# Performance work log

Measured on AMD Instinct MI355X. Metric: run time of the kernel, lower is better.

The kernel has to match this reference:

```python
import jax, jax.numpy as jnp
import numpy as np

H, D = 4, 32          # heads, per-head dim (= hidden_channels)
HD = H * D            # concat width fed between layers
L = 2                 # num HGT layers
OUT = 128             # final output dim
SCALE = 1.0 / np.sqrt(D)


def _seg_softmax(score, seg, n):
    # segment softmax over incoming edges per destination node, per head
    mx = jax.ops.segment_max(score, seg, num_segments=n)
    ex = jnp.exp(score - mx[seg])
    den = jax.ops.segment_sum(ex, seg, num_segments=n)
    return ex / den[seg]


def _hgt_side(q_dst, k_src, v_src, src, dst, a_rel, m_rel, p_rel, n_dst):
    # k/v: [N_src,H,D]; a_rel,m_rel: [H,D,D]; p_rel: [H]
    k_t = jnp.einsum('ehd,hdf->ehf', k_src[src], a_rel)          # [E,H,D]
    score = (q_dst[dst] * k_t).sum(-1) * p_rel * SCALE           # [E,H]
    alpha = _seg_softmax(score, dst, n_dst)                      # [E,H]
    v_t = jnp.einsum('ehd,hdf->ehf', v_src[src], m_rel)          # [E,H,D]
    return jax.ops.segment_sum(alpha[..., None] * v_t, dst, num_segments=n_dst)


def _forward(x_m, x_g, W_in_m, b_in_m, W_in_g, b_in_g,
             Wk_m, bk_m, Wq_m, bq_m, Wv_m, bv_m,
             Wk_g, bk_g, Wq_g, bq_g, Wv_g, bv_g,
             a_mg, m_mg, p_mg, a_gm, m_gm, p_gm,
             Wa_m, ba_m, Wa_g, ba_g, skip_m, skip_g,
             W_out_m, b_out_m, W_out_g, b_out_g,
             edge_mg_src, edge_mg_dst, edge_gm_src, edge_gm_dst):
    Nm, Ng = x_m.shape[0], x_g.shape[0]
    # per-node-type input projection
    h_m = x_m @ W_in_m + b_in_m                                  # [Nm,HD]
    h_g = x_g @ W_in_g + b_in_g                                  # [Ng,HD]
    for l in range(L):
        k_m = (h_m @ Wk_m[l] + bk_m[l]).reshape(Nm, H, D)
        q_m = (h_m @ Wq_m[l] + bq_m[l]).reshape(Nm, H, D)
        v_m = (h_m @ Wv_m[l] + bv_m[l]).reshape(Nm, H, D)
        k_g = (h_g @ Wk_g[l] + bk_g[l]).reshape(Ng, H, D)
        q_g = (h_g @ Wq_g[l] + bq_g[l]).reshape(Ng, H, D)
        v_g = (h_g @ Wv_g[l] + bv_g[l]).reshape(Ng, H, D)
        agg_g = _hgt_side(q_g, k_m, v_m, edge_mg_src, edge_mg_dst,
                          a_mg[l], m_mg[l], p_mg[l], Ng)         # [Ng,H,D]
        agg_m = _hgt_side(q_m, k_g, v_g, edge_gm_src, edge_gm_dst,
                          a_gm[l], m_gm[l], p_gm[l], Nm)         # [Nm,H,D]
        o_m = jax.nn.gelu(agg_m.reshape(Nm, HD), approximate=False) @ Wa_m[l] + ba_m[l]
        o_g = jax.nn.gelu(agg_g.reshape(Ng, HD), approximate=False) @ Wa_g[l] + ba_g[l]
        bm = jax.nn.sigmoid(skip_m[l])
        bg = jax.nn.sigmoid(skip_g[l])
        h_m = jax.nn.elu(bm * o_m + (1.0 - bm) * h_m)            # HGTConv skip, then model-level ELU
        h_g = jax.nn.elu(bg * o_g + (1.0 - bg) * h_g)
    out_m = h_m @ W_out_m + b_out_m                              # [Nm,OUT]
    out_g = h_g @ W_out_g + b_out_g                              # [Ng,OUT]
    return jnp.concatenate([out_m, out_g], axis=0)               # [Nm+Ng,OUT]


def setup_inputs() -> dict:
    key = jax.random.key(0)
    ks = iter(jax.random.split(key, 64))
    Nm, Ng, E = 100000, 20000, 500000
    Fm, Fg = 20, 50
    def n(shape, s=0.05):
        return jax.random.normal(next(ks), shape, jnp.float32) * s
    inp = {
        'x_m': n((Nm, Fm), 1.0), 'x_g': n((Ng, Fg), 1.0),
        'W_in_m': n((Fm, HD)), 'b_in_m': jnp.zeros((HD,), jnp.float32),
        'W_in_g': n((Fg, HD)), 'b_in_g': jnp.zeros((HD,), jnp.float32),
        'Wk_m': n((L, HD, HD)), 'bk_m': jnp.zeros((L, HD), jnp.float32),
        'Wq_m': n((L, HD, HD)), 'bq_m': jnp.zeros((L, HD), jnp.float32),
        'Wv_m': n((L, HD, HD)), 'bv_m': jnp.zeros((L, HD), jnp.float32),
        'Wk_g': n((L, HD, HD)), 'bk_g': jnp.zeros((L, HD), jnp.float32),
        'Wq_g': n((L, HD, HD)), 'bq_g': jnp.zeros((L, HD), jnp.float32),
        'Wv_g': n((L, HD, HD)), 'bv_g': jnp.zeros((L, HD), jnp.float32),
        'a_mg': n((L, H, D, D)), 'm_mg': n((L, H, D, D)),
        'p_mg': jnp.ones((L, H), jnp.float32),
        'a_gm': n((L, H, D, D)), 'm_gm': n((L, H, D, D)),
        'p_gm': jnp.ones((L, H), jnp.float32),
        'Wa_m': n((L, HD, HD)), 'ba_m': jnp.zeros((L, HD), jnp.float32),
        'Wa_g': n((L, HD, HD)), 'ba_g': jnp.zeros((L, HD), jnp.float32),
        'skip_m': jnp.ones((L,), jnp.float32), 'skip_g': jnp.ones((L,), jnp.float32),
        'W_out_m': n((HD, OUT)), 'b_out_m': jnp.zeros((OUT,), jnp.float32),
        'W_out_g': n((HD, OUT)), 'b_out_g': jnp.zeros((OUT,), jnp.float32),
        'edge_mg_src': jax.random.randint(next(ks), (E,), 0, Nm, jnp.int32),
        'edge_mg_dst': jax.random.randint(next(ks), (E,), 0, Ng, jnp.int32),
        'edge_gm_src': jax.random.randint(next(ks), (E,), 0, Ng, jnp.int32),
        'edge_gm_dst': jax.random.randint(next(ks), (E,), 0, Nm, jnp.int32),
    }
    return inp


def reference(x_m, x_g, W_in_m, b_in_m, W_in_g, b_in_g,
              Wk_m, bk_m, Wq_m, bq_m, Wv_m, bv_m,
              Wk_g, bk_g, Wq_g, bq_g, Wv_g, bv_g,
              a_mg, m_mg, p_mg, a_gm, m_gm, p_gm,
              Wa_m, ba_m, Wa_g, ba_g, skip_m, skip_g,
              W_out_m, b_out_m, W_out_g, b_out_g,
              edge_mg_src, edge_mg_dst, edge_gm_src, edge_gm_dst):
    return _forward(x_m, x_g, W_in_m, b_in_m, W_in_g, b_in_g,
                    Wk_m, bk_m, Wq_m, bq_m, Wv_m, bv_m,
                    Wk_g, bk_g, Wq_g, bq_g, Wv_g, bv_g,
                    a_mg, m_mg, p_mg, a_gm, m_gm, p_gm,
                    Wa_m, ba_m, Wa_g, ba_g, skip_m, skip_g,
                    W_out_m, b_out_m, W_out_g, b_out_g,
                    edge_mg_src, edge_mg_dst, edge_gm_src, edge_gm_dst)
```

## Files before the change

kernel.cpp:

```cpp
#include <hip/hip_runtime.h>
#include <hip/hip_bf16.h>

#define SCALE_F 0.17677669529663688f

typedef __attribute__((ext_vector_type(8)))  short bfrag;
typedef __attribute__((ext_vector_type(16))) float facc;
typedef __attribute__((ext_vector_type(2)))  float f32x2;

extern "C" __device__ float __ocml_native_exp2_f32(float);

__device__ __forceinline__ float lo16(unsigned u){ return __uint_as_float(u << 16); }
__device__ __forceinline__ float hi16(unsigned u){ return __uint_as_float(u & 0xffff0000u); }
__device__ __forceinline__ float bu2f(unsigned short u){ return __uint_as_float((unsigned)u << 16); }
__device__ __forceinline__ unsigned short f2bu(float f){
    __hip_bfloat16 h = __float2bfloat16(f);
    return *reinterpret_cast<unsigned short*>(&h);
}
__device__ __forceinline__ void storeC(float* p, float v){ *p = v; }
__device__ __forceinline__ void storeC(__hip_bfloat16* p, float v){ *p = __float2bfloat16(v); }

__global__ void hist2_k(const int* __restrict__ d1, int* __restrict__ c1, int E1, int N1,
                        const int* __restrict__ d2, int* __restrict__ c2, int E2, int N2){
    const int* d = blockIdx.y ? d2 : d1;
    int* c = blockIdx.y ? c2 : c1;
    int E = blockIdx.y ? E2 : E1;
    int Nd = blockIdx.y ? N2 : N1;
    int e = blockIdx.x*256 + threadIdx.x;
    if (e >= E) return;
    int dd = d[e];
    if ((unsigned)dd < (unsigned)Nd) atomicAdd(&c[dd], 1);
}

__global__ void scan_block2_k(const int* __restrict__ c1, int* __restrict__ i1, int* __restrict__ b1, int N1,
                              const int* __restrict__ c2, int* __restrict__ i2, int* __restrict__ b2, int N2){
    const int* cnt = blockIdx.y ? c2 : c1;
    int* incl = blockIdx.y ? i2 : i1;
    int* bsum = blockIdx.y ? b2 : b1;
    int N = blockIdx.y ? N2 : N1;
    if ((int)blockIdx.x*256 >= N) return;
    __shared__ int sh[256];
    int tid = threadIdx.x;
    int i = blockIdx.x*256 + tid;
    int v = (i < N) ? cnt[i] : 0;
    sh[tid] = v;
    __syncthreads();
    for (int off = 1; off < 256; off <<= 1){
        int t = (tid >= off) ? sh[tid-off] : 0;
        __syncthreads();
        sh[tid] += t;
        __syncthreads();
    }
    if (i < N) incl[i] = sh[tid];
    if (tid == 255) bsum[blockIdx.x] = sh[255];
}

__global__ void scan_top2_k(int* __restrict__ b1, int nb1, int* __restrict__ b2, int nb2){
    int* bsum = blockIdx.x ? b2 : b1;
    int nb = blockIdx.x ? nb2 : nb1;
    __shared__ int sh[512];
    int tid = threadIdx.x;
    int v = (tid < nb) ? bsum[tid] : 0;
    sh[tid] = v;
    __syncthreads();
    for (int off = 1; off < 512; off <<= 1){
        int t = (tid >= off) ? sh[tid-off] : 0;
        __syncthreads();
        sh[tid] += t;
        __syncthreads();
    }
    if (tid < nb) bsum[tid] = sh[tid] - v;
}

__global__ void finalize2_k(const int* __restrict__ i1, const int* __restrict__ c1,
                            const int* __restrict__ b1, int* __restrict__ p1, int N1, int E1,
                            const int* __restrict__ i2, const int* __restrict__ c2,
                            const int* __restrict__ b2, int* __restrict__ p2, int N2, int E2){
    const int* incl = blockIdx.y ? i2 : i1;
    const int* cnt  = blockIdx.y ? c2 : c1;
    const int* boff = blockIdx.y ? b2 : b1;
    int* indptr = blockIdx.y ? p2 : p1;
    int N = blockIdx.y ? N2 : N1;
    int E = blockIdx.y ? E2 : E1;
    int i = blockIdx.x*256 + threadIdx.x;
    if (i > N) return;
    if (i == N){ indptr[N] = E; return; }
    indptr[i] = boff[i >> 8] + incl[i] - cnt[i];
}

__global__ void scatter2_k(const int* __restrict__ s1, const int* __restrict__ d1,
                           const int* __restrict__ p1, int* __restrict__ u1,
                           int* __restrict__ r1, int E1, int N1,
                           const int* __restrict__ s2, const int* __restrict__ d2,
                           const int* __restrict__ p2, int* __restrict__ u2,
                           int* __restrict__ r2, int E2, int N2){
    const int* src = blockIdx.y ? s2 : s1;
    const int* dst = blockIdx.y ? d2 : d1;
    const int* indptr = blockIdx.y ? p2 : p1;
    int* cur = blockIdx.y ? u2 : u1;
    int* csr = blockIdx.y ? r2 : r1;
    int E = blockIdx.y ? E2 : E1;
    int Nd = blockIdx.y ? N2 : N1;
    int e = blockIdx.x*256 + threadIdx.x;
    if (e >= E) return;
    int d = dst[e];
    if ((unsigned)d >= (unsigned)Nd) return;
    int p = indptr[d] + atomicAdd(&cur[d], 1);
    csr[p] = src[e];
}

template<int K>
__device__ __forceinline__ void in_proj_body(const float* __restrict__ x,
                                             const float* __restrict__ W,
                                             const float* __restrict__ b,
                                             unsigned short* __restrict__ h, int N){
    constexpr int KP4 = (K + 3)/4, KP = KP4*4;
    int j = threadIdx.x;
    float wreg[KP];
    #pragma unroll
    for (int k = 0; k < KP; ++k) wreg[k] = (k < K) ? W[k*128 + j] : 0.f;
    float bj = b[j];
    __shared__ float xs[8][KP];
    for (int base = blockIdx.x*8; base < N; base += gridDim.x*8){
        __syncthreads();
        for (int t = threadIdx.x; t < 8*KP; t += 128){
            int r = t / KP, k = t - r*KP;
            int row = base + r;
            xs[r][k] = (row < N && k < K) ? x[(size_t)row*K + k] : 0.f;
        }
        __syncthreads();
        #pragma unroll
        for (int r = 0; r < 8; ++r){
            int row = base + r;
            if (row >= N) break;
            float acc = bj;
            #pragma unroll
            for (int kk = 0; kk < KP4; ++kk){
                float4 xv = *(const float4*)(&xs[r][kk*4]);
                acc += xv.x*wreg[kk*4] + xv.y*wreg[kk*4+1]
                     + xv.z*wreg[kk*4+2] + xv.w*wreg[kk*4+3];
            }
            h[(size_t)row*128 + j] = f2bu(acc);
        }
    }
}

__global__ __launch_bounds__(128) void in_proj2_k(
    const float* __restrict__ xm, const float* __restrict__ Wm,
    const float* __restrict__ bm_, unsigned short* __restrict__ hm, int Nm,
    const float* __restrict__ xg, const float* __restrict__ Wg,
    const float* __restrict__ bg_, unsigned short* __restrict__ hg, int Ng){
    if (blockIdx.y == 0) in_proj_body<20>(xm, Wm, bm_, hm, Nm);
    else                 in_proj_body<50>(xg, Wg, bg_, hg, Ng);
}

__global__ __launch_bounds__(128) void wprep_k(
    const float* __restrict__ Wq_m, const float* __restrict__ bq_m,
    const float* __restrict__ Wk_m, const float* __restrict__ bk_m,
    const float* __restrict__ Wv_m, const float* __restrict__ bv_m,
    const float* __restrict__ a_mg, const float* __restrict__ m_mg,
    const float* __restrict__ Wq_g, const float* __restrict__ bq_g,
    const float* __restrict__ Wk_g, const float* __restrict__ bk_g,
    const float* __restrict__ Wv_g, const float* __restrict__ bv_g,
    const float* __restrict__ a_gm, const float* __restrict__ m_gm,
    unsigned short* __restrict__ Wtf, float* __restrict__ bfv,
    const float* __restrict__ Wa_m, const float* __restrict__ Wa_g,
    const float* __restrict__ W_out_m, const float* __restrict__ W_out_g,
    unsigned short* __restrict__ Wta, unsigned short* __restrict__ Wtout){
    int b = blockIdx.x;
    if (b < 1536){
        int u = b / 384, j = b % 384;
        int l = u >> 1;  bool sg = (u & 1);
        const float* Wq = (sg ? Wq_g : Wq_m) + l*16384;
        const float* bq = (sg ? bq_g : bq_m) + l*128;
        const float* Wk = (sg ? Wk_g : Wk_m) + l*16384;
        const float* bk = (sg ? bk_g : bk_m) + l*128;
        const float* Wv = (sg ? Wv_g : Wv_m) + l*16384;
        const float* bv = (sg ? bv_g : bv_m) + l*128;
        const float* ar = (sg ? a_gm : a_mg) + l*4096;
        const float* mr = (sg ? m_gm : m_mg) + l*4096;
        unsigned short* Wt = Wtf + (size_t)u*49152;
        float* bf = bfv + u*384;
        int row = threadIdx.x;
        int part = j >> 7, f = j & 127, hh = f >> 5, ff = f & 31;
        float v;
        if (part == 0) v = Wq[row*128 + f];
        else {
            const float* Wx  = (part == 1) ? Wk : Wv;
            const float* rel = (part == 1) ? ar : mr;
            float s = 0.f;
            #pragma unroll
            for (int d = 0; d < 32; ++d)
                s += Wx[row*128 + hh*32 + d] * rel[hh*1024 + d*32 + ff];
            v = s;
        }
        Wt[(size_t)j*128 + row] = f2bu(v);
        if (row == 0){
            float bb;
            if (part == 0) bb = bq[f];
            else {
                const float* bx  = (part == 1) ? bk : bv;
                const float* rel = (part == 1) ? ar : mr;
                float s = 0.f;
                for (int d = 0; d < 32; ++d)
                    s += bx[hh*32 + d] * rel[hh*1024 + d*32 + ff];
                bb = s;
            }
            bf[j] = bb;
        }
    } else {
        int t = b - 1536;
        int y = t >> 7;
        int idx = (t & 127)*128 + threadIdx.x;
        const float* S = (y==0)?Wa_m:(y==1)?Wa_g:(y==2)?(Wa_m+16384):(y==3)?(Wa_g+16384)
                        :(y==4)?W_out_m:W_out_g;
        unsigned short* D = (y==0)?Wta:(y==1)?(Wta+16384):(y==2)?(Wta+32768):(y==3)?(Wta+49152)
                           :(y==4)?Wtout:(Wtout+16384);
        int n = idx >> 7, k = idx & 127;
        D[idx] = f2bu(S[k*128 + n]);
    }
}

template<typename CT, int MODE, int NCHUNK>
__global__ __launch_bounds__(256) void mfma_gemm2(
    const unsigned short* __restrict__ A0, const unsigned short* __restrict__ Wt0,
    const float* __restrict__ bias0, CT* __restrict__ C0, unsigned short* __restrict__ H0,
    int N0, const float* __restrict__ skip0,
    const unsigned short* __restrict__ A1, const unsigned short* __restrict__ Wt1,
    const float* __restrict__ bias1, CT* __restrict__ C1, unsigned short* __restrict__ H1,
    int N1, const float* __restrict__ skip1,
    int ldc, int nblk0){
    bool s0 = ((int)blockIdx.x < nblk0);
    const unsigned short* A  = s0 ? A0 : A1;
    const unsigned short* Wt = s0 ? Wt0 : Wt1;
    const float* bias = s0 ? bias0 : bias1;
    CT* C = s0 ? C0 : C1;
    unsigned short* H = s0 ? H0 : H1;
    int N = s0 ? N0 : N1;
    const float* skip = s0 ? skip0 : skip1;
    int bx = s0 ? blockIdx.x : (blockIdx.x - nblk0);

    __shared__ unsigned short As[64][136];
    __shared__ unsigned short Bs[128][136];
    int tid = threadIdx.x;
    int rb = bx*64;
    #pragma unroll
    for (int ph = 0; ph < 4; ++ph){
        int c = ph*256 + tid;
        int r = c >> 4, off = (c & 15)*8;
        uint4 v = make_uint4(0,0,0,0);
        if (rb + r < N) v = ((const uint4*)(A + (size_t)(rb + r)*128))[c & 15];
        *(uint4*)(&As[r][off]) = v;
    }
    int w = tid >> 6, lane = tid & 63;
    int wr = (w >> 1)*32, wc = (w & 1)*64;
    int m = lane & 31, quad = lane >> 5;
    const unsigned short* ap  = &As[wr + m][quad*8];
    const unsigned short* bp0 = &Bs[wc + m][quad*8];
    const unsigned short* bp1 = &Bs[wc + 32 + m][quad*8];
    float bm = 0.f;
    if (MODE == 2) bm = 1.f/(1.f + __expf(-skip[0]));

    #pragma unroll
    for (int chunk = 0; chunk < NCHUNK; ++chunk){
        int cb = chunk*128;
        if (chunk > 0) __syncthreads();
        #pragma unroll
        for (int ph = 0; ph < 8; ++ph){
            int c = ph*256 + tid;
            int r = c >> 4, off = (c & 15)*8;
            uint4 v = ((const uint4*)(Wt + (size_t)(cb + r)*128))[c & 15];
            *(uint4*)(&Bs[r][off]) = v;
        }
        __syncthreads();
        facc acc0, acc1;
        #pragma unroll
        for (int i = 0; i < 16; ++i){ acc0[i] = 0.f; acc1[i] = 0.f; }
        #pragma unroll
        for (int kc = 0; kc < 8; ++kc){
            bfrag a  = *(const bfrag*)(ap  + kc*16);
            bfrag b0 = *(const bfrag*)(bp0 + kc*16);
            bfrag b1 = *(const bfrag*)(bp1 + kc*16);
            acc0 = __builtin_amdgcn_mfma_f32_32x32x16_bf16(a, b0, acc0, 0, 0, 0);
            acc1 = __builtin_amdgcn_mfma_f32_32x32x16_bf16(a, b1, acc1, 0, 0, 0);
        }
        int col0 = cb + wc + m, col1 = col0 + 32;
        float bias0v = bias[col0], bias1v = bias[col1];
        #pragma unroll
        for (int r = 0; r < 16; ++r){
            int lrow = wr + 4*quad + (r & 3) + 8*(r >> 2);
            int grow = rb + lrow;
            if (grow >= N) continue;
            float o0 = acc0[r] + bias0v;
            float o1 = acc1[r] + bias1v;
            if (MODE == 0){
                storeC(&C[(size_t)grow*ldc + col0], o0);
                storeC(&C[(size_t)grow*ldc + col1], o1);
            } else if (MODE == 1){
                unsigned short* qp = (unsigned short*)C;
                if (col0 < 128){
                    qp[(size_t)grow*128 + col0] = f2bu(o0);
                    qp[(size_t)grow*128 + col1] = f2bu(o1);
                } else {
                    H[(size_t)grow*256 + (col0 - 128)] = f2bu(o0);
                    H[(size_t)grow*256 + (col1 - 128)] = f2bu(o1);
                }
            } else {
                size_t i0 = (size_t)grow*128 + col0, i1 = (size_t)grow*128 + col1;
                float v0 = bm*o0 + (1.f - bm)*bu2f(H[i0]);
                float v1 = bm*o1 + (1.f - bm)*bu2f(H[i1]);
                v0 = (v0 > 0.f) ? v0 : expm1f(v0);
                v1 = (v1 > 0.f) ? v1 : expm1f(v1);
                H[i0] = f2bu(v0);
                H[i1] = f2bu(v1);
            }
        }
    }
}

__global__ __launch_bounds__(256) void mfma_fused_mid_k(
    const unsigned short* __restrict__ A0, const unsigned short* __restrict__ Wt0,
    const float* __restrict__ bias0, unsigned short* __restrict__ H0,
    const float* __restrict__ skip0, const unsigned short* __restrict__ Wf0,
    const float* __restrict__ bf0, unsigned short* __restrict__ q0,
    unsigned short* __restrict__ kv0, int N0,
    const unsigned short* __restrict__ A1, const unsigned short* __restrict__ Wt1,
    const float* __restrict__ bias1, unsigned short* __restrict__ H1,
    const float* __restrict__ skip1, const unsigned short* __restrict__ Wf1,
    const float* __restrict__ bf1, unsigned short* __restrict__ q1,
    unsigned short* __restrict__ kv1, int N1,
    int nblk0){
    bool s0 = ((int)blockIdx.x < nblk0);
    const unsigned short* A  = s0 ? A0 : A1;
    const unsigned short* Wt = s0 ? Wt0 : Wt1;
    const float* bias = s0 ? bias0 : bias1;
    unsigned short* H = s0 ? H0 : H1;
    const float* skip = s0 ? skip0 : skip1;
    const unsigned short* Wf = s0 ? Wf0 : Wf1;
    const float* bf = s0 ? bf0 : bf1;
    unsigned short* q = s0 ? q0 : q1;
    unsigned short* kv = s0 ? kv0 : kv1;
    int N = s0 ? N0 : N1;
    int bx = s0 ? blockIdx.x : (blockIdx.x - nblk0);

    __shared__ unsigned short As[64][136];
    __shared__ unsigned short Bs[128][136];
    int tid = threadIdx.x;
    int rb = bx*64;
    #pragma unroll
    for (int ph = 0; ph < 4; ++ph){
        int c = ph*256 + tid;
        int r = c >> 4, off = (c & 15)*8;
        uint4 v = make_uint4(0,0,0,0);
        if (rb + r < N) v = ((const uint4*)(A + (size_t)(rb + r)*128))[c & 15];
        *(uint4*)(&As[r][off]) = v;
    }
    #pragma unroll
    for (int ph = 0; ph < 8; ++ph){
        int c = ph*256 + tid;
        int r = c >> 4, off = (c & 15)*8;
        uint4 v = ((const uint4*)(Wt + (size_t)r*128))[c & 15];
        *(uint4*)(&Bs[r][off]) = v;
    }
    __syncthreads();
    int w = tid >> 6, lane = tid & 63;
    int wr = (w >> 1)*32, wc = (w & 1)*64;
    int m = lane & 31, quad = lane >> 5;
    const unsigned short* ap  = &As[wr + m][quad*8];
    const unsigned short* bp0 = &Bs[wc + m][quad*8];
    const unsigned short* bp1 = &Bs[wc + 32 + m][quad*8];
    float bm = 1.f/(1.f + __expf(-skip[0]));

    facc acc0, acc1;
    #pragma unroll
    for (int i = 0; i < 16; ++i){ acc0[i] = 0.f; acc1[i] = 0.f; }
    #pragma unroll
    for (int kc = 0; kc < 8; ++kc){
        bfrag a  = *(const bfrag*)(ap  + kc*16);
        bfrag b0 = *(const bfrag*)(bp0 + kc*16);
        bfrag b1 = *(const bfrag*)(bp1 + kc*16);
        acc0 = __builtin_amdgcn_mfma_f32_32x32x16_bf16(a, b0, acc0, 0, 0, 0);
        acc1 = __builtin_amdgcn_mfma_f32_32x32x16_bf16(a, b1, acc1, 0, 0, 0);
    }
    __syncthreads();

    #pragma unroll
    for (int ph = 0; ph < 8; ++ph){
        int c = ph*256 + tid;
        int r = c >> 4, off = (c & 15)*8;
        uint4 v = ((const uint4*)(Wf + (size_t)r*128))[c & 15];
        *(uint4*)(&Bs[r][off]) = v;
    }
    {
        int col0 = wc + m, col1 = col0 + 32;
        float bias0v = bias[col0], bias1v = bias[col1];
        #pragma unroll
        for (int r = 0; r < 16; ++r){
            int lrow = wr + 4*quad + (r & 3) + 8*(r >> 2);
            int grow = rb + lrow;
            if (grow >= N) continue;
            float o0 = acc0[r] + bias0v;
            float o1 = acc1[r] + bias1v;
            size_t i0 = (size_t)grow*128 + col0, i1 = (size_t)grow*128 + col1;
            float v0 = bm*o0 + (1.f - bm)*bu2f(H[i0]);
            float v1 = bm*o1 + (1.f - bm)*bu2f(H[i1]);
            v0 = (v0 > 0.f) ? v0 : expm1f(v0);
            v1 = (v1 > 0.f) ? v1 : expm1f(v1);
            unsigned short h0 = f2bu(v0), h1 = f2bu(v1);
            H[i0] = h0;  H[i1] = h1;
            As[lrow][col0] = h0;
            As[lrow][col1] = h1;
        }
    }
    __syncthreads();

    #pragma unroll
    for (int chunk = 0; chunk < 3; ++chunk){
        if (chunk > 0){
            __syncthreads();
            #pragma unroll
            for (int ph = 0; ph < 8; ++ph){
                int c = ph*256 + tid;
                int r = c >> 4, off = (c & 15)*8;
                uint4 v = ((const uint4*)(Wf + (size_t)(chunk*128 + r)*128))[c & 15];
                *(uint4*)(&Bs[r][off]) = v;
            }
            __syncthreads();
        }
        facc qc0, qc1;
        #pragma unroll
        for (int i = 0; i < 16; ++i){ qc0[i] = 0.f; qc1[i] = 0.f; }
        #pragma unroll
        for (int kc = 0; kc < 8; ++kc){
            bfrag a  = *(const bfrag*)(ap  + kc*16);
            bfrag b0 = *(const bfrag*)(bp0 + kc*16);
            bfrag b1 = *(const bfrag*)(bp1 + kc*16);
            qc0 = __builtin_amdgcn_mfma_f32_32x32x16_bf16(a, b0, qc0, 0, 0, 0);
            qc1 = __builtin_amdgcn_mfma_f32_32x32x16_bf16(a, b1, qc1, 0, 0, 0);
        }
        int col0 = chunk*128 + wc + m, col1 = col0 + 32;
        float bf0v = bf[col0], bf1v = bf[col1];
        #pragma unroll
        for (int r = 0; r < 16; ++r){
            int lrow = wr + 4*quad + (r & 3) + 8*(r >> 2);
            int grow = rb + lrow;
            if (grow >= N) continue;
            float o0 = qc0[r] + bf0v;
            float o1 = qc1[r] + bf1v;
            if (col0 < 128){
                q[(size_t)grow*128 + col0] = f2bu(o0);
                q[(size_t)grow*128 + col1] = f2bu(o1);
            } else {
                kv[(size_t)grow*256 + (col0 - 128)] = f2bu(o0);
                kv[(size_t)grow*256 + (col1 - 128)] = f2bu(o1);
            }
        }
    }
}

__global__ __launch_bounds__(256) void mfma_fused_out_k(
    const unsigned short* __restrict__ A0, const unsigned short* __restrict__ Wt0,
    const float* __restrict__ bias0, const unsigned short* __restrict__ H0,
    const float* __restrict__ skip0, const unsigned short* __restrict__ Wo0,
    const float* __restrict__ bo0, float* __restrict__ O0, int N0,
    const unsigned short* __restrict__ A1, const unsigned short* __restrict__ Wt1,
    const float* __restrict__ bias1, const unsigned short* __restrict__ H1,
    const float* __restrict__ skip1, const unsigned short* __restrict__ Wo1,
    const float* __restrict__ bo1, float* __restrict__ O1, int N1,
    int nblk0){
    bool s0 = ((int)blockIdx.x < nblk0);
    const unsigned short* A  = s0 ? A0 : A1;
    const unsigned short* Wt = s0 ? Wt0 : Wt1;
    const float* bias = s0 ? bias0 : bias1;
    const unsigned short* H = s0 ? H0 : H1;
    const float* skip = s0 ? skip0 : skip1;
    const unsigned short* Wo = s0 ? Wo0 : Wo1;
    const float* bo = s0 ? bo0 : bo1;
    float* O = s0 ? O0 : O1;
    int N = s0 ? N0 : N1;
    int bx = s0 ? blockIdx.x : (blockIdx.x - nblk0);

    __shared__ unsigned short As[64][136];
    __shared__ unsigned short Bs[128][136];
    int tid = threadIdx.x;
    int rb = bx*64;
    #pragma unroll
    for (int ph = 0; ph < 4; ++ph){
        int c = ph*256 + tid;
        int r = c >> 4, off = (c & 15)*8;
        uint4 v = make_uint4(0,0,0,0);
        if (rb + r < N) v = ((const uint4*)(A + (size_t)(rb + r)*128))[c & 15];
        *(uint4*)(&As[r][off]) = v;
    }
    #pragma unroll
    for (int ph = 0; ph < 8; ++ph){
        int c = ph*256 + tid;
        int r = c >> 4, off = (c & 15)*8;
        uint4 v = ((const uint4*)(Wt + (size_t)r*128))[c & 15];
        *(uint4*)(&Bs[r][off]) = v;
    }
    __syncthreads();
    int w = tid >> 6, lane = tid & 63;
    int wr = (w >> 1)*32, wc = (w & 1)*64;
    int m = lane & 31, quad = lane >> 5;
    const unsigned short* ap  = &As[wr + m][quad*8];
    const unsigned short* bp0 = &Bs[wc + m][quad*8];
    const unsigned short* bp1 = &Bs[wc + 32 + m][quad*8];
    float bm = 1.f/(1.f + __expf(-skip[0]));

    facc acc0, acc1;
    #pragma unroll
    for (int i = 0; i < 16; ++i){ acc0[i] = 0.f; acc1[i] = 0.f; }
    #pragma unroll
    for (int kc = 0; kc < 8; ++kc){
        bfrag a  = *(const bfrag*)(ap  + kc*16);
        bfrag b0 = *(const bfrag*)(bp0 + kc*16);
        bfrag b1 = *(const bfrag*)(bp1 + kc*16);
        acc0 = __builtin_amdgcn_mfma_f32_32x32x16_bf16(a, b0, acc0, 0, 0, 0);
        acc1 = __builtin_amdgcn_mfma_f32_32x32x16_bf16(a, b1, acc1, 0, 0, 0);
    }
    __syncthreads();

    #pragma unroll
    for (int ph = 0; ph < 8; ++ph){
        int c = ph*256 + tid;
        int r = c >> 4, off = (c & 15)*8;
        uint4 v = ((const uint4*)(Wo + (size_t)r*128))[c & 15];
        *(uint4*)(&Bs[r][off]) = v;
    }
    int col0 = wc + m, col1 = col0 + 32;
    float bias0v = bias[col0], bias1v = bias[col1];
    #pragma unroll
    for (int r = 0; r < 16; ++r){
        int lrow = wr + 4*quad + (r & 3) + 8*(r >> 2);
        int grow = rb + lrow;
        if (grow >= N) continue;
        float o0 = acc0[r] + bias0v;
        float o1 = acc1[r] + bias1v;
        size_t i0 = (size_t)grow*128 + col0, i1 = (size_t)grow*128 + col1;
        float v0 = bm*o0 + (1.f - bm)*bu2f(H[i0]);
        float v1 = bm*o1 + (1.f - bm)*bu2f(H[i1]);
        v0 = (v0 > 0.f) ? v0 : expm1f(v0);
        v1 = (v1 > 0.f) ? v1 : expm1f(v1);
        As[lrow][col0] = f2bu(v0);
        As[lrow][col1] = f2bu(v1);
    }
    __syncthreads();

    facc oc0, oc1;
    #pragma unroll
    for (int i = 0; i < 16; ++i){ oc0[i] = 0.f; oc1[i] = 0.f; }
    #pragma unroll
    for (int kc = 0; kc < 8; ++kc){
        bfrag a  = *(const bfrag*)(ap  + kc*16);
        bfrag b0 = *(const bfrag*)(bp0 + kc*16);
        bfrag b1 = *(const bfrag*)(bp1 + kc*16);
        oc0 = __builtin_amdgcn_mfma_f32_32x32x16_bf16(a, b0, oc0, 0, 0, 0);
        oc1 = __builtin_amdgcn_mfma_f32_32x32x16_bf16(a, b1, oc1, 0, 0, 0);
    }
    float bo0v = bo[col0], bo1v = bo[col1];
    #pragma unroll
    for (int r = 0; r < 16; ++r){
        int lrow = wr + 4*quad + (r & 3) + 8*(r >> 2);
        int grow = rb + lrow;
        if (grow >= N) continue;
        O[(size_t)grow*128 + col0] = oc0[r] + bo0v;
        O[(size_t)grow*128 + col1] = oc1[r] + bo1v;
    }
}

__global__ __launch_bounds__(256) void edge_attn7_k(
    const int* __restrict__ ipA, const int* __restrict__ csrA,
    const unsigned short* __restrict__ qdA, const unsigned short* __restrict__ kvA,
    const float* __restrict__ pA, unsigned* __restrict__ aggA, int NdA,
    const int* __restrict__ ipB, const int* __restrict__ csrB,
    const unsigned short* __restrict__ qdB, const unsigned short* __restrict__ kvB,
    const float* __restrict__ pB, unsigned* __restrict__ aggB, int NdB,
    int nblkA){
    bool sA = ((int)blockIdx.x < nblkA);
    const int* ip  = sA ? ipA : ipB;
    const int* csr = sA ? csrA : csrB;
    const uint4* qd = (const uint4*)(sA ? qdA : qdB);
    const char* kvc = (const char*)(sA ? kvA : kvB);
    const float* p = sA ? pA : pB;
    unsigned* agg = sA ? aggA : aggB;
    int Nd = sA ? NdA : NdB;
    int bx = sA ? blockIdx.x : (blockIdx.x - nblkA);
    int wid  = (bx << 2) | (threadIdx.x >> 6);
    int lane = threadIdx.x & 63;
    if (wid >= Nd) return;
    int slot = lane >> 4, j = lane & 15;
    float phL = p[j >> 2] * (SCALE_F * 1.4426950408889634f);
    uint4 qv = qd[(size_t)wid*16 + j];
    f32x2 q2[4];
    q2[0] = (f32x2){lo16(qv.x), hi16(qv.x)};
    q2[1] = (f32x2){lo16(qv.y), hi16(qv.y)};
    q2[2] = (f32x2){lo16(qv.z), hi16(qv.z)};
    q2[3] = (f32x2){lo16(qv.w), hi16(qv.w)};
    int beg = ip[wid], end = ip[wid + 1];
    float den = 0.f;
    f32x2 acc2[4] = {};
    int loff = j*16;
    int i0 = beg + slot;
    if (i0 < end){
        int s0c = csr[i0];
        int i1 = i0 + 4;
        bool m1 = (i1 < end);
        int s1 = m1 ? csr[i1] : 0;
        const char* b0 = kvc + (size_t)s0c*512 + loff;
        uint4 kv = *(const uint4*)(b0);
        uint4 vv = *(const uint4*)(b0 + 256);
        while (true){
            int i2 = i1 + 4;
            bool m2 = (i2 < end);
            int s2 = m2 ? csr[i2] : 0;
            uint4 kv2, vv2;
            if (m1){
                const char* b1 = kvc + (size_t)s1*512 + loff;
                kv2 = *(const uint4*)(b1);
                vv2 = *(const uint4*)(b1 + 256);
            }
            f32x2 pp = q2[0] * (f32x2){lo16(kv.x), hi16(kv.x)};
            pp += q2[1] * (f32x2){lo16(kv.y), hi16(kv.y)};
            pp += q2[2] * (f32x2){lo16(kv.z), hi16(kv.z)};
            pp += q2[3] * (f32x2){lo16(kv.w), hi16(kv.w)};
            float part = pp.x + pp.y;
            part += __shfl_xor(part, 1);
            part += __shfl_xor(part, 2);
            float e = __ocml_native_exp2_f32(part * phL);
            den += e;
            acc2[0] += (f32x2){lo16(vv.x), hi16(vv.x)} * e;
            acc2[1] += (f32x2){lo16(vv.y), hi16(vv.y)} * e;
            acc2[2] += (f32x2){lo16(vv.z), hi16(vv.z)} * e;
            acc2[3] += (f32x2){lo16(vv.w), hi16(vv.w)} * e;
            if (!m1) break;
            kv = kv2; vv = vv2;
            i1 = i2; m1 = m2; s1 = s2;
        }
    }
    den += __shfl_xor(den, 16);
    den += __shfl_xor(den, 32);
    #pragma unroll
    for (int k = 0; k < 4; ++k){
        f32x2 t;
        t.x = __shfl_xor(acc2[k].x, 16);
        t.y = __shfl_xor(acc2[k].y, 16);
        acc2[k] += t;
        t.x = __shfl_xor(acc2[k].x, 32);
        t.y = __shfl_xor(acc2[k].y, 32);
        acc2[k] += t;
    }
    float inv = (den > 0.f) ? 1.f/den : 0.f;
    f32x2 sel = (slot & 2) ? ((slot & 1) ? acc2[3] : acc2[2])
                           : ((slot & 1) ? acc2[1] : acc2[0]);
    float o0 = sel.x*inv, o1 = sel.y*inv;
    o0 = 0.5f*o0*(1.f + erff(o0*0.70710678118654752f));
    o1 = 0.5f*o1*(1.f + erff(o1*0.70710678118654752f));
    agg[(size_t)wid*64 + j*4 + slot] = (unsigned)f2bu(o0) | ((unsigned)f2bu(o1) << 16);
}

extern "C" void kernel_launch(void* const* d_in, const int* in_sizes, int n_in,
                              void* d_out, int out_size, void* d_ws, size_t ws_size,
                              hipStream_t stream){
    typedef const float* FP;
    FP x_m = (FP)d_in[0], x_g = (FP)d_in[1];
    FP W_in_m = (FP)d_in[2], b_in_m = (FP)d_in[3], W_in_g = (FP)d_in[4], b_in_g = (FP)d_in[5];
    FP Wk_m = (FP)d_in[6],  bk_m = (FP)d_in[7],  Wq_m = (FP)d_in[8],  bq_m = (FP)d_in[9];
    FP Wv_m = (FP)d_in[10], bv_m = (FP)d_in[11];
    FP Wk_g = (FP)d_in[12], bk_g = (FP)d_in[13], Wq_g = (FP)d_in[14], bq_g = (FP)d_in[15];
    FP Wv_g = (FP)d_in[16], bv_g = (FP)d_in[17];
    FP a_mg = (FP)d_in[18], m_mg = (FP)d_in[19], p_mg = (FP)d_in[20];
    FP a_gm = (FP)d_in[21], m_gm = (FP)d_in[22], p_gm = (FP)d_in[23];
    FP Wa_m = (FP)d_in[24], ba_m = (FP)d_in[25], Wa_g = (FP)d_in[26], ba_g = (FP)d_in[27];
    FP skip_m = (FP)d_in[28], skip_g = (FP)d_in[29];
    FP W_out_m = (FP)d_in[30], b_out_m = (FP)d_in[31], W_out_g = (FP)d_in[32], b_out_g = (FP)d_in[33];
    const int* e_mg_src = (const int*)d_in[34];
    const int* e_mg_dst = (const int*)d_in[35];
    const int* e_gm_src = (const int*)d_in[36];
    const int* e_gm_dst = (const int*)d_in[37];

    const int Nm = in_sizes[0] / 20;
    const int Ng = in_sizes[1] / 50;
    const int E1 = in_sizes[34];
    const int E2 = in_sizes[36];

    char* wp = (char*)d_ws;
    auto alloc = [&](size_t bytes) -> char* {
        char* r = wp; wp += (bytes + 255) & ~(size_t)255; return r;
    };
    unsigned short* h_m   = (unsigned short*)alloc((size_t)Nm*128*2);
    unsigned short* h_g   = (unsigned short*)alloc((size_t)Ng*128*2);
    unsigned short* agg_m = (unsigned short*)alloc((size_t)Nm*128*2);
    unsigned short* agg_g = (unsigned short*)alloc((size_t)Ng*128*2);
    unsigned short* q_m   = (unsigned short*)alloc((size_t)Nm*128*2);
    unsigned short* kv_m  = (unsigned short*)alloc((size_t)Nm*256*2);
    unsigned short* q_g   = (unsigned short*)alloc((size_t)Ng*128*2);
    unsigned short* kv_g  = (unsigned short*)alloc((size_t)Ng*256*2);
    unsigned short* Wtf   = (unsigned short*)alloc((size_t)4*49152*2);
    float*          bfv   = (float*)alloc((size_t)4*384*4);
    unsigned short* Wta   = (unsigned short*)alloc((size_t)4*16384*2);
    unsigned short* Wtout = (unsigned short*)alloc((size_t)2*16384*2);
    int* indptr_g = (int*)alloc((size_t)(Ng+1)*4);
    int* csr_mg   = (int*)alloc((size_t)E1*4);
    int* indptr_m = (int*)alloc((size_t)(Nm+1)*4);
    int* csr_gm   = (int*)alloc((size_t)E2*4);
    int maxN = Nm > Ng ? Nm : Ng;
    int* cnt  = (int*)alloc((size_t)maxN*4);
    int* cur  = (int*)alloc((size_t)maxN*4);
    int* cnt2 = (int*)alloc((size_t)maxN*4);
    int* cur2 = (int*)alloc((size_t)maxN*4);
    int* incl = (int*)alloc((size_t)maxN*4);
    int* incl2= (int*)alloc((size_t)maxN*4);
    int* bsum = (int*)alloc(512*4);
    int* bsum2= (int*)alloc(512*4);

    size_t used = (size_t)(wp - (char*)d_ws);
    if (used > ws_size){
        hipMemsetAsync(d_out, 0, (size_t)out_size*4, stream);
        return;
    }
    hipMemsetAsync(cnt, 0, (size_t)((char*)cur2 - (char*)cnt) + (size_t)maxN*4, stream);

    int maxE = E1 > E2 ? E1 : E2;
    int nb1 = (Ng + 255)/256, nb2 = (Nm + 255)/256;
    int nbmax = nb1 > nb2 ? nb1 : nb2;
    hist2_k<<<dim3((maxE + 255)/256, 2), 256, 0, stream>>>(
        e_mg_dst, cnt, E1, Ng, e_gm_dst, cnt2, E2, Nm);
    scan_block2_k<<<dim3(nbmax, 2), 256, 0, stream>>>(
        cnt, incl, bsum, Ng, cnt2, incl2, bsum2, Nm);
    scan_top2_k<<<2, 512, 0, stream>>>(bsum, nb1, bsum2, nb2);
    finalize2_k<<<dim3(nbmax + 1, 2), 256, 0, stream>>>(
        incl, cnt, bsum, indptr_g, Ng, E1, incl2, cnt2, bsum2, indptr_m, Nm, E2);
    scatter2_k<<<dim3((maxE + 255)/256, 2), 256, 0, stream>>>(
        e_mg_src, e_mg_dst, indptr_g, cur, csr_mg, E1, Ng,
        e_gm_src, e_gm_dst, indptr_m, cur2, csr_gm, E2, Nm);

    wprep_k<<<2304, 128, 0, stream>>>(
        Wq_m, bq_m, Wk_m, bk_m, Wv_m, bv_m, a_mg, m_mg,
        Wq_g, bq_g, Wk_g, bk_g, Wv_g, bv_g, a_gm, m_gm,
        Wtf, bfv, Wa_m, Wa_g, W_out_m, W_out_g, Wta, Wtout);

    in_proj2_k<<<dim3(2048, 2), 128, 0, stream>>>(
        x_m, W_in_m, b_in_m, h_m, Nm,
        x_g, W_in_g, b_in_g, h_g, Ng);

    int gxm = (Nm + 63)/64, gxg = (Ng + 63)/64;
    int nbA = (Ng + 3)/4, nbB = (Nm + 3)/4;

    float* outp = (float*)d_out;

    mfma_gemm2<__hip_bfloat16, 1, 3><<<dim3(gxm + gxg, 1), 256, 0, stream>>>(
        h_m, Wtf + (size_t)0*49152, bfv + 0*384,
        (__hip_bfloat16*)q_m, kv_m, Nm, nullptr,
        h_g, Wtf + (size_t)1*49152, bfv + 1*384,
        (__hip_bfloat16*)q_g, kv_g, Ng, nullptr,
        0, gxm);

    edge_attn7_k<<<nbA + nbB, 256, 0, stream>>>(
        indptr_g, csr_mg, q_g, kv_m, p_mg + 0, (unsigned*)agg_g, Ng,
        indptr_m, csr_gm, q_m, kv_g, p_gm + 0, (unsigned*)agg_m, Nm,
        nbA);

    mfma_fused_mid_k<<<dim3(gxm + gxg, 1), 256, 0, stream>>>(
        agg_m, Wta + (size_t)0*16384, ba_m + 0, h_m, skip_m + 0,
        Wtf + (size_t)2*49152, bfv + 2*384, q_m, kv_m, Nm,
        agg_g, Wta + (size_t)1*16384, ba_g + 0, h_g, skip_g + 0,
        Wtf + (size_t)3*49152, bfv + 3*384, q_g, kv_g, Ng,
        gxm);

    edge_attn7_k<<<nbA + nbB, 256, 0, stream>>>(
        indptr_g, csr_mg, q_g, kv_m, p_mg + 4, (unsigned*)agg_g, Ng,
        indptr_m, csr_gm, q_m, kv_g, p_gm + 4, (unsigned*)agg_m, Nm,
        nbA);

    mfma_fused_out_k<<<dim3(gxm + gxg, 1), 256, 0, stream>>>(
        agg_m, Wta + (size_t)2*16384, ba_m + 128, h_m, skip_m + 1,
        Wtout, b_out_m, outp, Nm,
        agg_g, Wta + (size_t)3*16384, ba_g + 128, h_g, skip_g + 1,
        Wtout + 16384, b_out_g, outp + (size_t)Nm*128, Ng,
        gxm);
}
```

Before: 574.2 us.

## Fuse input projection into first-layer QKV MFMA GEMM kernel

Removes the separate input-projection kernel and computes each 64-row tile of h directly in the QKV GEMM kernel. The tile is staged in shared memory as the A operand and still written to global for later skip connections. This saves one launch and the reload of h from global. In exchange each block loads the input weights into registers and does serial FMA work before its MFMA phase, and the x staging buffer reuses the B shared-memory region.

Result: no change. 580.7 us (+1.1%).

```diff
diff --git a/kernel.cpp b/kernel.cpp
--- a/kernel.cpp
+++ b/kernel.cpp
@@ -106,51 +106,6 @@
     if ((unsigned)d >= (unsigned)Nd) return;
     int p = indptr[d] + atomicAdd(&cur[d], 1);
     csr[p] = src[e];
-}
-
-template<int K>
-__device__ __forceinline__ void in_proj_body(const float* __restrict__ x,
-                                             const float* __restrict__ W,
-                                             const float* __restrict__ b,
-                                             unsigned short* __restrict__ h, int N){
-    constexpr int KP4 = (K + 3)/4, KP = KP4*4;
-    int j = threadIdx.x;
-    float wreg[KP];
-    #pragma unroll
-    for (int k = 0; k < KP; ++k) wreg[k] = (k < K) ? W[k*128 + j] : 0.f;
-    float bj = b[j];
-    __shared__ float xs[8][KP];
-    for (int base = blockIdx.x*8; base < N; base += gridDim.x*8){
-        __syncthreads();
-        for (int t = threadIdx.x; t < 8*KP; t += 128){
-            int r = t / KP, k = t - r*KP;
-            int row = base + r;
-            xs[r][k] = (row < N && k < K) ? x[(size_t)row*K + k] : 0.f;
-        }
-        __syncthreads();
-        #pragma unroll
-        for (int r = 0; r < 8; ++r){
-            int row = base + r;
-            if (row >= N) break;
-            float acc = bj;
-            #pragma unroll
-            for (int kk = 0; kk < KP4; ++kk){
-                float4 xv = *(const float4*)(&xs[r][kk*4]);
-                acc += xv.x*wreg[kk*4] + xv.y*wreg[kk*4+1]
-                     + xv.z*wreg[kk*4+2] + xv.w*wreg[kk*4+3];
-            }
-            h[(size_t)row*128 + j] = f2bu(acc);
-        }
-    }
-}
-
-__global__ __launch_bounds__(128) void in_proj2_k(
-    const float* __restrict__ xm, const float* __restrict__ Wm,
-    const float* __restrict__ bm_, unsigned short* __restrict__ hm, int Nm,
-    const float* __restrict__ xg, const float* __restrict__ Wg,
-    const float* __restrict__ bg_, unsigned short* __restrict__ hg, int Ng){
-    if (blockIdx.y == 0) in_proj_body<20>(xm, Wm, bm_, hm, Nm);
-    else                 in_proj_body<50>(xg, Wg, bg_, hg, Ng);
 }
 
 __global__ __launch_bounds__(128) void wprep_k(
@@ -312,6 +267,118 @@
                 v1 = (v1 > 0.f) ? v1 : expm1f(v1);
                 H[i0] = f2bu(v0);
                 H[i1] = f2bu(v1);
+            }
+        }
+    }
+}
+
+template<int K>
+__device__ __forceinline__ void inproj_tile(
+    const float* __restrict__ x, const float* __restrict__ Win,
+    const float* __restrict__ bin, unsigned short* __restrict__ H,
+    float* xs, unsigned short (*As)[136], int rb, int N, int tid){
+    constexpr int KP4 = (K + 3)/4, KP = KP4*4;
+    for (int t = tid; t < 64*KP; t += 256){
+        int r = t / KP, k = t - r*KP;
+        int row = rb + r;
+        xs[r*KP + k] = (row < N && k < K) ? x[(size_t)row*K + k] : 0.f;
+    }
+    __syncthreads();
+    int j = tid & 127, half = tid >> 7;
+    float wreg[KP];
+    #pragma unroll
+    for (int k = 0; k < KP; ++k) wreg[k] = (k < K) ? Win[k*128 + j] : 0.f;
+    float bj = bin[j];
+    #pragma unroll
+    for (int r = 0; r < 32; ++r){
+        int lrow = half*32 + r;
+        float acc = bj;
+        #pragma unroll
+        for (int kk = 0; kk < KP4; ++kk){
+            float4 xv = *(const float4*)(&xs[lrow*KP + kk*4]);
+            acc += xv.x*wreg[kk*4] + xv.y*wreg[kk*4+1]
+                 + xv.z*wreg[kk*4+2] + xv.w*wreg[kk*4+3];
+        }
+        unsigned short hv = f2bu(acc);
+        As[lrow][j] = hv;
+        int grow = rb + lrow;
+        if (grow < N) H[(size_t)grow*128 + j] = hv;
+    }
+}
+
+__global__ __launch_bounds__(256) void mfma_fused_in_k(
+    const float* __restrict__ x0, const float* __restrict__ Wi0,
+    const float* __restrict__ bi0, unsigned short* __restrict__ H0,
+    const unsigned short* __restrict__ Wf0, const float* __restrict__ bf0,
+    unsigned short* __restrict__ q0, unsigned short* __restrict__ kv0, int N0,
+    const float* __restrict__ x1, const float* __restrict__ Wi1,
+    const float* __restrict__ bi1, unsigned short* __restrict__ H1,
+    const unsigned short* __restrict__ Wf1, const float* __restrict__ bf1,
+    unsigned short* __restrict__ q1, unsigned short* __restrict__ kv1, int N1,
+    int nblk0){
+    bool s0 = ((int)blockIdx.x < nblk0);
+    const unsigned short* Wf = s0 ? Wf0 : Wf1;
+    const float* bf = s0 ? bf0 : bf1;
+    unsigned short* q = s0 ? q0 : q1;
+    unsigned short* kv = s0 ? kv0 : kv1;
+    int N = s0 ? N0 : N1;
+    int bx = s0 ? blockIdx.x : (blockIdx.x - nblk0);
+
+    __shared__ __align__(16) unsigned short As[64][136];
+    __shared__ __align__(16) unsigned short Bs[128][136];
+    float* xs = (float*)&Bs[0][0];
+    int tid = threadIdx.x;
+    int rb = bx*64;
+
+    if (s0) inproj_tile<20>(x0, Wi0, bi0, H0, xs, As, rb, N, tid);
+    else    inproj_tile<50>(x1, Wi1, bi1, H1, xs, As, rb, N, tid);
+    __syncthreads();
+
+    int w = tid >> 6, lane = tid & 63;
+    int wr = (w >> 1)*32, wc = (w & 1)*64;
+    int m = lane & 31, quad = lane >> 5;
+    const unsigned short* ap  = &As[wr + m][quad*8];
+    const unsigned short* bp0 = &Bs[wc + m][quad*8];
+    const unsigned short* bp1 = &Bs[wc + 32 + m][quad*8];
+
+    #pragma unroll
+    for (int chunk = 0; chunk < 3; ++chunk){
+        int cb = chunk*128;
+        if (chunk > 0) __syncthreads();
+        #pragma unroll
+        for (int ph = 0; ph < 8; ++ph){
+            int c = ph*256 + tid;
+            int r = c >> 4, off = (c & 15)*8;
+            uint4 v = ((const uint4*)(Wf + (size_t)(cb + r)*128))[c & 15];
+            *(uint4*)(&Bs[r][off]) = v;
+        }
+        __syncthreads();
+        facc acc0, acc1;
+        #pragma unroll
+        for (int i = 0; i < 16; ++i){ acc0[i] = 0.f; acc1[i] = 0.f; }
+        #pragma unroll
+        for (int kc = 0; kc < 8; ++kc){
+            bfrag a  = *(const bfrag*)(ap  + kc*16);
+            bfrag b0 = *(const bfrag*)(bp0 + kc*16);
+            bfrag b1 = *(const bfrag*)(bp1 + kc*16);
+            acc0 = __builtin_amdgcn_mfma_f32_32x32x16_bf16(a, b0, acc0, 0, 0, 0);
+            acc1 = __builtin_amdgcn_mfma_f32_32x32x16_bf16(a, b1, acc1, 0, 0, 0);
+        }
+        int col0 = cb + wc + m, col1 = col0 + 32;
+        float bf0v = bf[col0], bf1v = bf[col1];
+        #pragma unroll
+        for (int r = 0; r < 16; ++r){
+            int lrow = wr + 4*quad + (r & 3) + 8*(r >> 2);
+            int grow = rb + lrow;
+            if (grow >= N) continue;
+            float o0 = acc0[r] + bf0v;
+            float o1 = acc1[r] + bf1v;
+            if (col0 < 128){
+                q[(size_t)grow*128 + col0] = f2bu(o0);
+                q[(size_t)grow*128 + col1] = f2bu(o1);
+            } else {
+                kv[(size_t)grow*256 + (col0 - 128)] = f2bu(o0);
+                kv[(size_t)grow*256 + (col1 - 128)] = f2bu(o1);
             }
         }
     }
@@ -739,21 +806,15 @@
         Wq_g, bq_g, Wk_g, bk_g, Wv_g, bv_g, a_gm, m_gm,
         Wtf, bfv, Wa_m, Wa_g, W_out_m, W_out_g, Wta, Wtout);
 
-    in_proj2_k<<<dim3(2048, 2), 128, 0, stream>>>(
-        x_m, W_in_m, b_in_m, h_m, Nm,
-        x_g, W_in_g, b_in_g, h_g, Ng);
-
     int gxm = (Nm + 63)/64, gxg = (Ng + 63)/64;
     int nbA = (Ng + 3)/4, nbB = (Nm + 3)/4;
 
     float* outp = (float*)d_out;
 
-    mfma_gemm2<__hip_bfloat16, 1, 3><<<dim3(gxm + gxg, 1), 256, 0, stream>>>(
-        h_m, Wtf + (size_t)0*49152, bfv + 0*384,
-        (__hip_bfloat16*)q_m, kv_m, Nm, nullptr,
-        h_g, Wtf + (size_t)1*49152, bfv + 1*384,
-        (__hip_bfloat16*)q_g, kv_g, Ng, nullptr,
-        0, gxm);
+    mfma_fused_in_k<<<dim3(gxm + gxg, 1), 256, 0, stream>>>(
+        x_m, W_in_m, b_in_m, h_m, Wtf + (size_t)0*49152, bfv + 0*384, q_m, kv_m, Nm,
+        x_g, W_in_g, b_in_g, h_g, Wtf + (size_t)1*49152, bfv + 1*384, q_g, kv_g, Ng,
+        gxm);
 
     edge_attn7_k<<<nbA + nbB, 256, 0, stream>>>(
         indptr_g, csr_mg, q_g, kv_m, p_mg + 0, (unsigned*)agg_g, Ng,
```
